# Optimization experiments

Hardware: AMD Instinct MI355X
Metric: run time of the kernel (lower is better)

## Reference

```python
import jax, jax.numpy as jnp
import numpy as np

B_SZ, L_SEQ = 8, 2048
D_MODEL, N_STATE = 1024, 64
NUM_HEADS, N_REC = 1, 8
H_DIM = D_MODEL // NUM_HEADS


def setup_inputs() -> dict:
    key = jax.random.key(0)
    ks = jax.random.split(key, 12)
    Np = N_STATE
    return {
        "u": jax.random.normal(ks[0], (B_SZ, L_SEQ, D_MODEL), jnp.float32),
        "k_proj_w": jax.random.normal(ks[1], (D_MODEL, D_MODEL), jnp.float32) / np.float32(np.sqrt(D_MODEL)),
        "k_proj_b": jax.random.normal(ks[2], (D_MODEL,), jnp.float32) * 0.02,
        "shift_B": jax.random.normal(ks[3], (D_MODEL, Np), jnp.float32) / np.float32(np.sqrt(Np)),
        "shift_C": jax.random.normal(ks[4], (D_MODEL, Np), jnp.float32) / np.float32(np.sqrt(Np)),
        "ssm_k_D": jax.random.normal(ks[5], (D_MODEL,), jnp.float32),
        "log_dt": jax.random.uniform(ks[6], (H_DIM,), jnp.float32, minval=np.float32(np.log(1e-3)), maxval=np.float32(np.log(1e-1))),
        "log_A_real": jnp.log(0.5 * jnp.ones((H_DIM, Np), jnp.float32)),
        "A_imag": jnp.broadcast_to(np.float32(np.pi) * jnp.arange(Np, dtype=jnp.float32), (H_DIM, Np)),
        "B_re": jax.random.normal(ks[7], (H_DIM, Np), jnp.float32),
        "B_im": jax.random.normal(ks[8], (H_DIM, Np), jnp.float32),
    }


def _shift_kernel(Bp, Cp, L):
    # Shift-SSM kernel (SSKernel mode='shift'): K(l) = sum_m C[m+l] * B[m], zero for l >= N.
    N = Bp.shape[-1]
    nfft = 2 * N
    Bf = jnp.fft.rfft(Bp, n=nfft)
    Cf = jnp.fft.rfft(Cp, n=nfft)
    k = jnp.fft.irfft(Cf * jnp.conj(Bf), n=nfft)[..., :N]  # (D, N) linear cross-correlation
    return jnp.pad(k, ((0, 0), (0, L - N)))  # (D, L)


def _kernel_expand(k, log_dt, log_A_real, A_imag, B_re, B_im):
    # Diagonal-SSM state expansion: SSM states x_t = sum_{s<=t} dA^{t-s} dB u_s,
    # read out at N_REC evenly spaced chunk boundaries.
    # k: (B, G, H, L) real -> (B, N_REC, G, H, N) real
    Bb, G, H, L = k.shape
    Lc = L // N_REC
    dt = jnp.exp(log_dt)[:, None]                      # (H,1)
    A = -jnp.exp(log_A_real) + 1j * A_imag             # (H,N)
    dA_log = dt * A                                    # (H,N)
    dB = (B_re + 1j * B_im) * ((jnp.exp(dA_log) - 1.0) / A)  # ZOH discretization
    exps = jnp.arange(Lc - 1, -1, -1, dtype=jnp.float32)      # (Lc,)
    P = jnp.exp(dA_log[..., None] * exps) * dB[..., None]     # (H,N,Lc): dA^{Lc-1-i} dB
    kc = k.reshape(Bb, G, H, N_REC, Lc).astype(P.dtype)
    contrib = jnp.einsum('hnl,bghrl->rbghn', P, kc)           # (N_REC,B,G,H,N)
    dA_Lc = jnp.exp(dA_log * Lc)                              # (H,N)
    x0 = jnp.zeros((Bb, G, H, A.shape[-1]), P.dtype)

    def step(x, c):
        x = dA_Lc * x + c
        return x, x

    _, states = jax.lax.scan(step, x0, contrib)               # (N_REC,B,G,H,N)
    return jnp.transpose(states.real, (1, 0, 2, 3, 4))


def reference(u, k_proj_w, k_proj_b, shift_B, shift_C, ssm_k_D, log_dt, log_A_real, A_imag, B_re, B_im):
    Bb, L, D = u.shape
    # k = W @ u^T + b  -> (B, D, L)
    k = jnp.einsum('bld,hd->bhl', u, k_proj_w) + k_proj_b[None, :, None]
    Ks = _shift_kernel(shift_B, shift_C, L)  # (D, L)
    nfft = 2 * L  # fft_size = L_kernel + L
    conv = jnp.fft.irfft(jnp.fft.rfft(Ks, n=nfft)[None] * jnp.fft.rfft(k, n=nfft), n=nfft)[..., :L]
    k = conv + ssm_k_D[None, :, None] * k
    # rearrange 'b (h d1) l -> b d1 h l'
    k = k.reshape(Bb, H_DIM, NUM_HEADS, L).transpose(0, 2, 1, 3)
    return _kernel_expand(k, log_dt, log_A_real, A_imag, B_re, B_im)
```

## Files before the change

kernel.cpp:

```cpp
#include <hip/hip_runtime.h>
#include <cstddef>
#include <cstdint>

#define L_SEQ 2048
#define DM    1024
#define NREC  8
#define BM 128
#define BN 128
#define BK 32
#define NT (DM / BK)

typedef __attribute__((ext_vector_type(8))) short short8;
typedef __attribute__((ext_vector_type(4))) float f32x4;
typedef __attribute__((ext_vector_type(2))) unsigned int u32x2;

__device__ inline unsigned short f2bf(float f) {
    unsigned u = __float_as_uint(f);
    unsigned r = (u + 0x7FFFu + ((u >> 16) & 1u)) >> 16;
    return (unsigned short)r;
}
__device__ inline float bf2f(unsigned short s) {
    return __uint_as_float(((unsigned)s) << 16);
}
__device__ inline void gload_lds16(const void* g, void* l) {
    __builtin_amdgcn_global_load_lds(
        (const __attribute__((address_space(1))) void*)g,
        (__attribute__((address_space(3))) void*)l, 16, 0, 0);
}

__global__ __launch_bounds__(256) void cvt2_bf16(
    const float* __restrict__ a, unsigned short* __restrict__ oa, int na,
    const float* __restrict__ b, unsigned short* __restrict__ ob, int nb)
{
    int i = (blockIdx.x * 256 + threadIdx.x) * 8;
    const float* src;
    unsigned short* dst;
    if (i < na) { src = a + i; dst = oa + i; }
    else {
        int j = i - na;
        if (j >= nb) return;
        src = b + j; dst = ob + j;
    }
    f32x4 v0 = *(const f32x4*)(src);
    f32x4 v1 = *(const f32x4*)(src + 4);
    short8 o;
    o[0] = (short)f2bf(v0[0]); o[1] = (short)f2bf(v0[1]);
    o[2] = (short)f2bf(v0[2]); o[3] = (short)f2bf(v0[3]);
    o[4] = (short)f2bf(v1[0]); o[5] = (short)f2bf(v1[1]);
    o[6] = (short)f2bf(v1[2]); o[7] = (short)f2bf(v1[3]);
    *(short8*)dst = o;
}

template<bool PREW>
__global__ __launch_bounds__(256, 2) void gemm_klin(
    const float* __restrict__ Wf, const unsigned short* __restrict__ Wb,
    const unsigned short* __restrict__ ub,
    const float* __restrict__ bias, unsigned short* __restrict__ klin)
{
    __shared__ unsigned short As[2][BM * BK];
    __shared__ unsigned short Bs[2][BM * BK];
    int wg = (int)blockIdx.x;
    wg = (wg & 7) * 128 + (wg >> 3);
    const int b  = wg >> 7;
    const int h0 = ((wg >> 4) & 7) * BM;
    const int l0 = (wg & 15) * BN;
    const int tid = threadIdx.x;
    const int lane = tid & 63, wv = tid >> 6;

    const int l3 = lane >> 3, l7 = lane & 7;
    const int g  = l7 ^ l3;
    const int rij  = l3 * 2 + (g >> 2);
    const int kcol = (g & 3) * 8;

    const int rA0 = 2 * wv * 16 + rij;
    const unsigned short* gA0b = Wb + (size_t)(h0 + rA0) * DM + kcol;
    const unsigned short* gA1b = gA0b + 16 * DM;
    const unsigned short* gB0 = ub + ((size_t)(b * L_SEQ + l0 + rA0)) * DM + kcol;
    const unsigned short* gB1 = gB0 + 16 * DM;

    const int r0 = wv * 32 + (lane >> 2);
    const int r1 = r0 + 16;
    const int slotF = lane & 3;
    const float* gA0f = Wf + (size_t)(h0 + r0) * DM + slotF * 8;
    const float* gA1f = Wf + (size_t)(h0 + r1) * DM + slotF * 8;
    const int w0off = (r0 >> 1) * 128 + ((((r0 & 1) << 2) + slotF) ^ ((r0 >> 1) & 7)) * 16;
    const int w1off = (r1 >> 1) * 128 + ((((r1 & 1) << 2) + slotF) ^ ((r1 >> 1) & 7)) * 16;

    const int wm = wv >> 1, wn = wv & 1;
    const int lr = lane & 15, lk = lane >> 4;
    const int foff = (lr >> 1) * 128 + ((((lr & 1) << 2) + lk) ^ (lr >> 1)) * 16;

    f32x4 acc[4][4];
    #pragma unroll
    for (int m = 0; m < 4; ++m)
        #pragma unroll
        for (int n = 0; n < 4; ++n) acc[m][n] = (f32x4){0.f, 0.f, 0.f, 0.f};

    gload_lds16(gB0, &Bs[0][(2 * wv) * 512]);
    gload_lds16(gB1, &Bs[0][(2 * wv + 1) * 512]);
    if constexpr (PREW) {
        gload_lds16(gA0b, &As[0][(2 * wv) * 512]);
        gload_lds16(gA1b, &As[0][(2 * wv + 1) * 512]);
    } else {
        f32x4 a0 = *(const f32x4*)(gA0f);
        f32x4 a1 = *(const f32x4*)(gA0f + 4);
        f32x4 a2 = *(const f32x4*)(gA1f);
        f32x4 a3 = *(const f32x4*)(gA1f + 4);
        short8 c0, c1;
        c0[0]=(short)f2bf(a0[0]); c0[1]=(short)f2bf(a0[1]); c0[2]=(short)f2bf(a0[2]); c0[3]=(short)f2bf(a0[3]);
        c0[4]=(short)f2bf(a1[0]); c0[5]=(short)f2bf(a1[1]); c0[6]=(short)f2bf(a1[2]); c0[7]=(short)f2bf(a1[3]);
        c1[0]=(short)f2bf(a2[0]); c1[1]=(short)f2bf(a2[1]); c1[2]=(short)f2bf(a2[2]); c1[3]=(short)f2bf(a2[3]);
        c1[4]=(short)f2bf(a3[0]); c1[5]=(short)f2bf(a3[1]); c1[6]=(short)f2bf(a3[2]); c1[7]=(short)f2bf(a3[3]);
        *(short8*)((char*)&As[0][0] + w0off) = c0;
        *(short8*)((char*)&As[0][0] + w1off) = c1;
    }

    for (int kt = 0; kt < NT; ++kt) {
        __syncthreads();
        const int bf = kt & 1;
        const bool more = (kt + 1 < NT);
        f32x4 a0, a1, a2, a3;
        if (more) {
            const int ko = (kt + 1) * BK;
            gload_lds16(gB0 + ko, &Bs[bf ^ 1][(2 * wv) * 512]);
            gload_lds16(gB1 + ko, &Bs[bf ^ 1][(2 * wv + 1) * 512]);
            if constexpr (PREW) {
                gload_lds16(gA0b + ko, &As[bf ^ 1][(2 * wv) * 512]);
                gload_lds16(gA1b + ko, &As[bf ^ 1][(2 * wv + 1) * 512]);
            } else {
                a0 = *(const f32x4*)(gA0f + ko);
                a1 = *(const f32x4*)(gA0f + ko + 4);
                a2 = *(const f32x4*)(gA1f + ko);
                a3 = *(const f32x4*)(gA1f + ko + 4);
            }
        }
        short8 af[4], bfr[4];
        #pragma unroll
        for (int m = 0; m < 4; ++m) {
            const int rb = wm * 64 + m * 16;
            af[m] = *(const short8*)((const char*)&As[bf][0] + rb * 64 + foff);
        }
        #pragma unroll
        for (int n = 0; n < 4; ++n) {
            const int rb = wn * 64 + n * 16;
            bfr[n] = *(const short8*)((const char*)&Bs[bf][0] + rb * 64 + foff);
        }
        #pragma unroll
        for (int m = 0; m < 4; ++m)
            #pragma unroll
            for (int n = 0; n < 4; ++n)
                acc[m][n] = __builtin_amdgcn_mfma_f32_16x16x32_bf16(af[m], bfr[n], acc[m][n], 0, 0, 0);
        if constexpr (!PREW) {
            if (more) {
                short8 c0, c1;
                c0[0]=(short)f2bf(a0[0]); c0[1]=(short)f2bf(a0[1]); c0[2]=(short)f2bf(a0[2]); c0[3]=(short)f2bf(a0[3]);
                c0[4]=(short)f2bf(a1[0]); c0[5]=(short)f2bf(a1[1]); c0[6]=(short)f2bf(a1[2]); c0[7]=(short)f2bf(a1[3]);
                c1[0]=(short)f2bf(a2[0]); c1[1]=(short)f2bf(a2[1]); c1[2]=(short)f2bf(a2[2]); c1[3]=(short)f2bf(a2[3]);
                c1[4]=(short)f2bf(a3[0]); c1[5]=(short)f2bf(a3[1]); c1[6]=(short)f2bf(a3[2]); c1[7]=(short)f2bf(a3[3]);
                *(short8*)((char*)&As[bf ^ 1][0] + w0off) = c0;
                *(short8*)((char*)&As[bf ^ 1][0] + w1off) = c1;
            }
        }
    }

    #pragma unroll
    for (int m = 0; m < 4; ++m) {
        const int h = h0 + wm * 64 + m * 16 + lk * 4;
        #pragma unroll
        for (int n = 0; n < 4; ++n) {
            const int l = l0 + wn * 64 + n * 16 + lr;
            #pragma unroll
            for (int r = 0; r < 4; ++r) {
                float v = acc[m][n][r] + bias[h + r];
                klin[((size_t)b * DM + h + r) * L_SEQ + l] = f2bf(v);
            }
        }
    }
}

__device__ inline void get_disc(const float* __restrict__ log_dt,
                                const float* __restrict__ lar,
                                const float* __restrict__ aim, int h, int n,
                                float& Are, float& Aim, float& lre, float& lim)
{
    float dtv = expf(log_dt[h]);
    Are = -expf(lar[h * 64 + n]);
    Aim = aim[h * 64 + n];
    lre = dtv * Are;
    lim = dtv * Aim;
}

__global__ __launch_bounds__(256, 5) void expand(
    const unsigned short* __restrict__ klin,
    const float* __restrict__ shift_B, const float* __restrict__ shift_C,
    const float* __restrict__ ssm_k_D, const float* __restrict__ log_dt,
    const float* __restrict__ log_A_real, const float* __restrict__ A_imag,
    const float* __restrict__ B_re, const float* __restrict__ B_im,
    float* __restrict__ out)
{
    __shared__ __align__(16) char sm[29696];
    constexpr int OKL = 0;
    constexpr int OKK = 8704;
    constexpr int OAF = 16896;
    constexpr int OPR = 20224;
    constexpr int OPI = 24320;
    constexpr int OF  = 28416;
    constexpr int OBS = 28672;
    constexpr int OCS = 28928;
    constexpr int OW32 = 29184;

    const int h  = blockIdx.x;
    const int bg = blockIdx.y;
    const int t = threadIdx.x;
    const int lane = t & 63, wv = t >> 6;

    if (t < 32) {
        int rl = t >> 4, reg = (t >> 3) & 1, idx = t & 7;
        *(f32x4*)&sm[OKL + rl * 4352 + reg * 4224 + idx * 16] = (f32x4){0.f, 0.f, 0.f, 0.f};
    }
    {
        const int rl = wv >> 1, hf = wv & 1;
        const int b = bg * 2 + rl;
        const char* krow = (const char*)(klin + ((size_t)b * DM + h) * L_SEQ);
        const int s = (2 * rl + 1 + (lane >> 3)) & 7;
        const int so = hf * 2048 + (lane >> 3) * 128 + ((lane ^ s) & 7) * 16;
        gload_lds16(krow + so,        &sm[OKL + rl * 4352 + 128 + hf * 2048]);
        gload_lds16(krow + so + 1024, &sm[OKL + rl * 4352 + 128 + hf * 2048 + 1024]);
    }
    if (t < 64) {
        ((float*)&sm[OBS])[t] = shift_B[h * 64 + t];
        ((float*)&sm[OCS])[t] = shift_C[h * 64 + t];
        float Are, Aim, lre, lim;
        get_disc(log_dt, log_A_real, A_imag, h, t, Are, Aim, lre, lim);
        float er = expf(32.f * lre);
        float sn, cs; sincosf(32.f * lim, &sn, &cs);
        ((float*)&sm[OW32])[t * 2]     = er * cs;
        ((float*)&sm[OW32])[t * 2 + 1] = er * sn;
    }
    {
        int n = t >> 2, s4 = t & 3;
        float Are, Aim, lre, lim;
        get_disc(log_dt, log_A_real, A_imag, h, n, Are, Aim, lre, lim);
        float erw = expf(lre), snw, csw;
        sincosf(lim, &snw, &csw);
        float wr = erw * csw, wi = erw * snw;
        float e0 = (float)(24 - 8 * s4);
        float mag = expf(e0 * lre);
        float sn0, cs0; sincosf(e0 * lim, &sn0, &cs0);
        float pr = mag * cs0, pi = mag * sn0;
        float vr[8], vi[8];
        vr[7] = pr; vi[7] = pi;
        #pragma unroll
        for (int k = 6; k >= 0; --k) {
            float nr = pr * wr - pi * wi;
            pi = fmaf(pr, wi, pi * wr);
            pr = nr;
            vr[k] = pr; vi[k] = pi;
        }
        short8 re8, im8;
        #pragma unroll
        for (int e = 0; e < 8; ++e) {
            re8[e] = (short)f2bf(vr[e]);
            im8[e] = (short)f2bf(vi[e]);
        }
        *(short8*)&sm[OPR + t * 16] = re8;
        *(short8*)&sm[OPI + t * 16] = im8;
    }
    __syncthreads();

    if (t < 64) {
        const float* Bp = (const float*)&sm[OBS];
        const float* Cp = (const float*)&sm[OCS];
        float f = (t == 0) ? ssm_k_D[h] : 0.f;
        #pragma unroll 8
        for (int j = 0; j < 64; ++j) {
            float cv = Cp[(j + t) & 63];
            f = fmaf((j + t < 64) ? cv : 0.f, Bp[j], f);
        }
        ((float*)&sm[OF])[t] = f;
    }
    __syncthreads();

    {
        int i = t >> 4, ks = t & 15;
        if (ks < 12) {
            const float* Fp = (const float*)&sm[OF];
            short8 row;
            #pragma unroll
            for (int e = 0; e < 8; ++e) {
                int k = ks * 8 + e;
                int m = 64 + i - k;
                float v = (m >= 0 && m < 64) ? Fp[m] : 0.f;
                row[e] = (short)f2bf(v);
            }
            *(short8*)&sm[OAF + i * 208 + ks * 16] = row;
        }
    }
    __syncthreads();

    {
        short8 afr[3];
        #pragma unroll
        for (int ks = 0; ks < 3; ++ks)
            afr[ks] = *(const short8*)&sm[OAF + (lane & 15) * 208 + ks * 64 + (lane >> 4) * 16];
        const int rl = wv >> 1;
        const int jbase = (wv & 1) * 4;
        #pragma unroll
        for (int jj = 0; jj < 4; ++jj) {
            const int jg = jbase + jj;
            f32x4 d = (f32x4){0.f, 0.f, 0.f, 0.f};
            #pragma unroll
            for (int ks = 0; ks < 3; ++ks) {
                int o = rl * 4352 + (jg * 256 + (lane & 15) * 16 + ks * 32 + (lane >> 4) * 8) * 2;
                o ^= ((o >> 7) & 7) << 4;
                short8 bfrag = *(const short8*)&sm[OKL + o];
                d = __builtin_amdgcn_mfma_f32_16x16x32_bf16(afr[ks], bfrag, d, 0, 0, 0);
            }
            unsigned pk0 = ((unsigned)f2bf(d[0])) | (((unsigned)f2bf(d[1])) << 16);
            unsigned pk1 = ((unsigned)f2bf(d[2])) | (((unsigned)f2bf(d[3])) << 16);
            int o2 = rl * 4096 + jg * 512 + (lane & 15) * 32 + (lane >> 4) * 8;
            o2 ^= ((o2 >> 9) & 7) << 4;
            *(u32x2*)&sm[OKK + o2] = (u32x2){pk0, pk1};
        }
    }
    __syncthreads();

    {
        const int mt = wv;
        short8 par = *(const short8*)&sm[OPR + (mt * 16 + (lane & 15)) * 64 + (lane >> 4) * 16];
        short8 pai = *(const short8*)&sm[OPI + (mt * 16 + (lane & 15)) * 64 + (lane >> 4) * 16];
        float w32r[4], w32i[4];
        #pragma unroll
        for (int rg = 0; rg < 4; ++rg) {
            int n = mt * 16 + (lane >> 4) * 4 + rg;
            float2 ww = *(const float2*)&sm[OW32 + n * 8];
            w32r[rg] = ww.x;
            w32i[rg] = ww.y;
        }
        f32x4 cr = (f32x4){0.f, 0.f, 0.f, 0.f};
        f32x4 ci_ = (f32x4){0.f, 0.f, 0.f, 0.f};
        const int colb = (lane & 15) >> 3;
        const int colr = lane & 7;
        #pragma unroll
        for (int g2 = 0; g2 < 8; ++g2) {
            int o = colb * 4096 + colr * 512 + g2 * 64 + (lane >> 4) * 16;
            o ^= ((o >> 9) & 7) << 4;
            short8 kf = *(const short8*)&sm[OKK + o];
            f32x4 sre = __builtin_amdgcn_mfma_f32_16x16x32_bf16(par, kf, (f32x4){0.f,0.f,0.f,0.f}, 0, 0, 0);
            f32x4 sim = __builtin_amdgcn_mfma_f32_16x16x32_bf16(pai, kf, (f32x4){0.f,0.f,0.f,0.f}, 0, 0, 0);
            #pragma unroll
            for (int rg = 0; rg < 4; ++rg) {
                float wr = w32r[rg], wi = w32i[rg];
                float ncr = fmaf(cr[rg], wr, fmaf(-ci_[rg], wi, sre[rg]));
                float nci = fmaf(cr[rg], wi, fmaf(ci_[rg], wr, sim[rg]));
                cr[rg] = ncr;
                ci_[rg] = nci;
            }
        }
        __syncthreads();
        #pragma unroll
        for (int rg = 0; rg < 4; ++rg) {
            int n = mt * 16 + (lane >> 4) * 4 + rg;
            int c = lane & 15;
            ((float*)&sm[OKK])[n * 17 + c] = cr[rg];
            ((float*)&sm[OKK])[1088 + n * 17 + c] = ci_[rg];
        }
    }
    __syncthreads();

    if (t < 128) {
        const int n = t & 63, bl = t >> 6;
        const int b = bg * 2 + bl;
        float Are, Aim, lre, lim;
        get_disc(log_dt, log_A_real, A_imag, h, n, Are, Aim, lre, lim);
        float er = expf(lre), sn, cs;
        sincosf(lim, &sn, &cs);
        float wr = er * cs, wi = er * sn;
        float2 w32v = *(const float2*)&sm[OW32 + n * 8];
        float ar = w32v.x, ai = w32v.y;
        #pragma unroll
        for (int s = 0; s < 3; ++s) {
            float nr = ar * ar - ai * ai;
            ai = 2.f * ar * ai;
            ar = nr;
        }
        float den = Are * Are + Aim * Aim;
        float wm1r = wr - 1.f, wm1i = wi;
        float tr_ = (wm1r * Are + wm1i * Aim) / den;
        float ti_ = (wm1i * Are - wm1r * Aim) / den;
        float br = B_re[h * 64 + n], bi = B_im[h * 64 + n];
        float dBr = br * tr_ - bi * ti_;
        float dBi = br * ti_ + bi * tr_;
        const float* cre = (const float*)&sm[OKK] + n * 17 + bl * 8;
        const float* cim = (const float*)&sm[OKK] + 1088 + n * 17 + bl * 8;
        float sr = 0.f, si_ = 0.f;
        #pragma unroll
        for (int r = 0; r < 8; ++r) {
            float nsr = fmaf(ar, sr, fmaf(-ai, si_, cre[r]));
            float nsi = fmaf(ar, si_, fmaf(ai, sr, cim[r]));
            sr = nsr; si_ = nsi;
            out[(((size_t)b * NREC + r) * DM + h) * 64 + n] = dBr * sr - dBi * si_;
        }
    }
}

extern "C" void kernel_launch(void* const* d_in, const int* in_sizes, int n_in,
                              void* d_out, int out_size, void* d_ws, size_t ws_size,
                              hipStream_t stream)
{
    const float* u       = (const float*)d_in[0];
    const float* W       = (const float*)d_in[1];
    const float* bias    = (const float*)d_in[2];
    const float* shift_B = (const float*)d_in[3];
    const float* shift_C = (const float*)d_in[4];
    const float* ssm_k_D = (const float*)d_in[5];
    const float* log_dt  = (const float*)d_in[6];
    const float* log_Ar  = (const float*)d_in[7];
    const float* A_imag  = (const float*)d_in[8];
    const float* B_re    = (const float*)d_in[9];
    const float* B_im    = (const float*)d_in[10];
    float* out = (float*)d_out;

    const int n_u = 8 * L_SEQ * DM;
    const int n_w = DM * DM;
    unsigned short* ub   = (unsigned short*)d_ws;
    unsigned short* klin = ub + (size_t)n_u;
    unsigned short* Wb   = klin + (size_t)n_u;

    const bool prew = ws_size >= (size_t)66 * 1024 * 1024;

    if (prew) {
        cvt2_bf16<<<(n_u + n_w) / (256 * 8), 256, 0, stream>>>(u, ub, n_u, W, Wb, n_w);
        gemm_klin<true><<<dim3(1024), 256, 0, stream>>>(W, Wb, ub, bias, klin);
    } else {
        cvt2_bf16<<<n_u / (256 * 8), 256, 0, stream>>>(u, ub, n_u, W, Wb, 0);
        gemm_klin<false><<<dim3(1024), 256, 0, stream>>>(W, Wb, ub, bias, klin);
    }

    expand<<<dim3(DM, 4), 256, 0, stream>>>(klin, shift_B, shift_C, ssm_k_D, log_dt,
                                            log_Ar, A_imag, B_re, B_im, out);
}
```

Before: 87.53 us.

## Add 256x256-tile 8-wave GEMM with 4-stage LDS pipeline for projection

Replaces the 128x128 tile, 4-wave, double-buffered bf16 GEMM with a 256x256 tile, 512-thread kernel. The new kernel uses a four-buffer LDS ring with loads issued three tiles ahead, explicit vmcnt waits and barriers, and s_setprio around the MFMA blocks. Larger tiles raise reuse per loaded byte and the deeper pipeline hides global latency. In exchange, only 256 workgroups launch (one wave of CUs), with 128 KB of LDS and higher register pressure per block. The fallback path for a small workspace is kept as a separate fp32-W kernel.

Measured after the change: 81.88 us. -6.4%, faster.

```diff
diff --git a/kernel.cpp b/kernel.cpp
--- a/kernel.cpp
+++ b/kernel.cpp
@@ -51,9 +51,117 @@
     *(short8*)dst = o;
 }
 
-template<bool PREW>
-__global__ __launch_bounds__(256, 2) void gemm_klin(
-    const float* __restrict__ Wf, const unsigned short* __restrict__ Wb,
+__global__ __launch_bounds__(512, 2) void gemm_klin8(
+    const unsigned short* __restrict__ Wb,
+    const unsigned short* __restrict__ ub,
+    const float* __restrict__ bias, unsigned short* __restrict__ klin)
+{
+    __shared__ unsigned short As[4][256 * 32];
+    __shared__ unsigned short Bs[4][256 * 32];
+
+    int wg = (int)blockIdx.x;
+    wg = (wg & 7) * 32 + (wg >> 3);
+    const int b  = wg >> 5;
+    const int l0 = ((wg >> 2) & 7) * 256;
+    const int h0 = (wg & 3) * 256;
+    const int tid = (int)threadIdx.x;
+    const int lane = tid & 63, wv = tid >> 6;
+
+    const int l3 = lane >> 3, l7 = lane & 7;
+    const int gsw  = l7 ^ l3;
+    const int rij  = l3 * 2 + (gsw >> 2);
+    const int kcol = (gsw & 3) * 8;
+    const int rA0  = wv * 16 + rij;
+
+    const unsigned short* gA0 = Wb + (size_t)(h0 + rA0) * DM + kcol;
+    const unsigned short* gA1 = gA0 + (size_t)128 * DM;
+    const unsigned short* gB0 = ub + ((size_t)b * L_SEQ + l0 + rA0) * DM + kcol;
+    const unsigned short* gB1 = gB0 + (size_t)128 * DM;
+    const int dst0 = (wv * 8) * 128;
+    const int dst1 = (64 + wv * 8) * 128;
+
+    const int wm = wv >> 2, wn = wv & 3;
+    const int lr = lane & 15, lk = lane >> 4;
+    const int foff = (lr >> 1) * 128 + ((((lr & 1) << 2) + lk) ^ (lr >> 1)) * 16;
+
+    f32x4 acc[8][4];
+    #pragma unroll
+    for (int mf = 0; mf < 8; ++mf)
+        #pragma unroll
+        for (int nf = 0; nf < 4; ++nf) acc[mf][nf] = (f32x4){0.f, 0.f, 0.f, 0.f};
+
+#define STG_A(T, BUF) do { const int ko_ = (T) * 32; \
+    gload_lds16(gA0 + ko_, (char*)&As[BUF][0] + dst0); \
+    gload_lds16(gA1 + ko_, (char*)&As[BUF][0] + dst1); } while (0)
+#define STG_B(T, BUF) do { const int ko_ = (T) * 32; \
+    gload_lds16(gB0 + ko_, (char*)&Bs[BUF][0] + dst0); \
+    gload_lds16(gB1 + ko_, (char*)&Bs[BUF][0] + dst1); } while (0)
+
+    STG_A(0, 0); STG_B(0, 0);
+    STG_A(1, 1); STG_B(1, 1);
+    STG_A(2, 2); STG_B(2, 2);
+    asm volatile("s_waitcnt vmcnt(8)" ::: "memory");
+    __builtin_amdgcn_s_barrier();
+    asm volatile("" ::: "memory");
+
+    #pragma unroll 1
+    for (int t = 0; t < 32; ++t) {
+        const int cur = t & 3, st = (t + 3) & 3;
+        const char* Ab = (const char*)&As[cur][0];
+        const char* Bb = (const char*)&Bs[cur][0];
+        short8 af[4], bfr[4];
+        #pragma unroll
+        for (int nf = 0; nf < 4; ++nf)
+            bfr[nf] = *(const short8*)(Bb + (wn * 64 + nf * 16) * 64 + foff);
+        #pragma unroll
+        for (int mf = 0; mf < 4; ++mf)
+            af[mf] = *(const short8*)(Ab + (wm * 128 + mf * 16) * 64 + foff);
+        if (t + 3 < 32) STG_A(t + 3, st);
+        __builtin_amdgcn_s_setprio(1);
+        #pragma unroll
+        for (int mf = 0; mf < 4; ++mf)
+            #pragma unroll
+            for (int nf = 0; nf < 4; ++nf)
+                acc[mf][nf] = __builtin_amdgcn_mfma_f32_16x16x32_bf16(af[mf], bfr[nf], acc[mf][nf], 0, 0, 0);
+        __builtin_amdgcn_s_setprio(0);
+        #pragma unroll
+        for (int mf = 0; mf < 4; ++mf)
+            af[mf] = *(const short8*)(Ab + (wm * 128 + (mf + 4) * 16) * 64 + foff);
+        if (t + 3 < 32) STG_B(t + 3, st);
+        __builtin_amdgcn_s_setprio(1);
+        #pragma unroll
+        for (int mf = 0; mf < 4; ++mf)
+            #pragma unroll
+            for (int nf = 0; nf < 4; ++nf)
+                acc[mf + 4][nf] = __builtin_amdgcn_mfma_f32_16x16x32_bf16(af[mf], bfr[nf], acc[mf + 4][nf], 0, 0, 0);
+        __builtin_amdgcn_s_setprio(0);
+        if (t <= 28)      asm volatile("s_waitcnt vmcnt(8)" ::: "memory");
+        else if (t == 29) asm volatile("s_waitcnt vmcnt(4)" ::: "memory");
+        else              asm volatile("s_waitcnt vmcnt(0)" ::: "memory");
+        __builtin_amdgcn_s_barrier();
+        asm volatile("" ::: "memory");
+        __builtin_amdgcn_sched_barrier(0);
+    }
+#undef STG_A
+#undef STG_B
+
+    #pragma unroll
+    for (int mf = 0; mf < 8; ++mf) {
+        const int h = h0 + wm * 128 + mf * 16 + lk * 4;
+        #pragma unroll
+        for (int nf = 0; nf < 4; ++nf) {
+            const int l = l0 + wn * 64 + nf * 16 + lr;
+            #pragma unroll
+            for (int r = 0; r < 4; ++r) {
+                float v = acc[mf][nf][r] + bias[h + r];
+                klin[((size_t)b * DM + h + r) * L_SEQ + l] = f2bf(v);
+            }
+        }
+    }
+}
+
+__global__ __launch_bounds__(256, 2) void gemm_klin_fb(
+    const float* __restrict__ Wf,
     const unsigned short* __restrict__ ub,
     const float* __restrict__ bias, unsigned short* __restrict__ klin)
 {
@@ -71,10 +179,7 @@
     const int g  = l7 ^ l3;
     const int rij  = l3 * 2 + (g >> 2);
     const int kcol = (g & 3) * 8;
-
     const int rA0 = 2 * wv * 16 + rij;
-    const unsigned short* gA0b = Wb + (size_t)(h0 + rA0) * DM + kcol;
-    const unsigned short* gA1b = gA0b + 16 * DM;
     const unsigned short* gB0 = ub + ((size_t)(b * L_SEQ + l0 + rA0)) * DM + kcol;
     const unsigned short* gB1 = gB0 + 16 * DM;
 
@@ -98,10 +203,7 @@
 
     gload_lds16(gB0, &Bs[0][(2 * wv) * 512]);
     gload_lds16(gB1, &Bs[0][(2 * wv + 1) * 512]);
-    if constexpr (PREW) {
-        gload_lds16(gA0b, &As[0][(2 * wv) * 512]);
-        gload_lds16(gA1b, &As[0][(2 * wv + 1) * 512]);
-    } else {
+    {
         f32x4 a0 = *(const f32x4*)(gA0f);
         f32x4 a1 = *(const f32x4*)(gA0f + 4);
         f32x4 a2 = *(const f32x4*)(gA1f);
@@ -124,15 +226,10 @@
             const int ko = (kt + 1) * BK;
             gload_lds16(gB0 + ko, &Bs[bf ^ 1][(2 * wv) * 512]);
             gload_lds16(gB1 + ko, &Bs[bf ^ 1][(2 * wv + 1) * 512]);
-            if constexpr (PREW) {
-                gload_lds16(gA0b + ko, &As[bf ^ 1][(2 * wv) * 512]);
-                gload_lds16(gA1b + ko, &As[bf ^ 1][(2 * wv + 1) * 512]);
-            } else {
-                a0 = *(const f32x4*)(gA0f + ko);
-                a1 = *(const f32x4*)(gA0f + ko + 4);
-                a2 = *(const f32x4*)(gA1f + ko);
-                a3 = *(const f32x4*)(gA1f + ko + 4);
-            }
+            a0 = *(const f32x4*)(gA0f + ko);
+            a1 = *(const f32x4*)(gA0f + ko + 4);
+            a2 = *(const f32x4*)(gA1f + ko);
+            a3 = *(const f32x4*)(gA1f + ko + 4);
         }
         short8 af[4], bfr[4];
         #pragma unroll
@@ -150,16 +247,14 @@
             #pragma unroll
             for (int n = 0; n < 4; ++n)
                 acc[m][n] = __builtin_amdgcn_mfma_f32_16x16x32_bf16(af[m], bfr[n], acc[m][n], 0, 0, 0);
-        if constexpr (!PREW) {
-            if (more) {
-                short8 c0, c1;
-                c0[0]=(short)f2bf(a0[0]); c0[1]=(short)f2bf(a0[1]); c0[2]=(short)f2bf(a0[2]); c0[3]=(short)f2bf(a0[3]);
-                c0[4]=(short)f2bf(a1[0]); c0[5]=(short)f2bf(a1[1]); c0[6]=(short)f2bf(a1[2]); c0[7]=(short)f2bf(a1[3]);
-                c1[0]=(short)f2bf(a2[0]); c1[1]=(short)f2bf(a2[1]); c1[2]=(short)f2bf(a2[2]); c1[3]=(short)f2bf(a2[3]);
-                c1[4]=(short)f2bf(a3[0]); c1[5]=(short)f2bf(a3[1]); c1[6]=(short)f2bf(a3[2]); c1[7]=(short)f2bf(a3[3]);
-                *(short8*)((char*)&As[bf ^ 1][0] + w0off) = c0;
-                *(short8*)((char*)&As[bf ^ 1][0] + w1off) = c1;
-            }
+        if (more) {
+            short8 c0, c1;
+            c0[0]=(short)f2bf(a0[0]); c0[1]=(short)f2bf(a0[1]); c0[2]=(short)f2bf(a0[2]); c0[3]=(short)f2bf(a0[3]);
+            c0[4]=(short)f2bf(a1[0]); c0[5]=(short)f2bf(a1[1]); c0[6]=(short)f2bf(a1[2]); c0[7]=(short)f2bf(a1[3]);
+            c1[0]=(short)f2bf(a2[0]); c1[1]=(short)f2bf(a2[1]); c1[2]=(short)f2bf(a2[2]); c1[3]=(short)f2bf(a2[3]);
+            c1[4]=(short)f2bf(a3[0]); c1[5]=(short)f2bf(a3[1]); c1[6]=(short)f2bf(a3[2]); c1[7]=(short)f2bf(a3[3]);
+            *(short8*)((char*)&As[bf ^ 1][0] + w0off) = c0;
+            *(short8*)((char*)&As[bf ^ 1][0] + w1off) = c1;
         }
     }
 
@@ -431,10 +526,10 @@
 
     if (prew) {
         cvt2_bf16<<<(n_u + n_w) / (256 * 8), 256, 0, stream>>>(u, ub, n_u, W, Wb, n_w);
-        gemm_klin<true><<<dim3(1024), 256, 0, stream>>>(W, Wb, ub, bias, klin);
+        gemm_klin8<<<dim3(256), 512, 0, stream>>>(Wb, ub, bias, klin);
     } else {
         cvt2_bf16<<<n_u / (256 * 8), 256, 0, stream>>>(u, ub, n_u, W, Wb, 0);
-        gemm_klin<false><<<dim3(1024), 256, 0, stream>>>(W, Wb, ub, bias, klin);
+        gemm_klin_fb<<<dim3(1024), 256, 0, stream>>>(W, ub, bias, klin);
     }
 
     expand<<<dim3(DM, 4), 256, 0, stream>>>(klin, shift_B, shift_C, ssm_k_D, log_dt,
```

## Fuse fp32-to-bf16 conversion into GEMM with larger 256x256 tiles

Applied to the files above, without the earlier changes.

Removes the separate conversion kernel that wrote a bf16 copy of u and W, and instead loads fp32 directly in the GEMM, packing to bf16 in registers before storing to LDS. The GEMM tile grows to 256x256 with 512 threads and 256 blocks, and the MFMA phases are wrapped in s_setprio. This removes a full read/write pass over u, but the GEMM now reads twice the bytes per element from global memory. With only 256 blocks and higher register use, occupancy may not cover all CUs well.

After: 78.16 us. 10.7% less time.

```diff
diff --git a/kernel.cpp b/kernel.cpp
--- a/kernel.cpp
+++ b/kernel.cpp
@@ -5,10 +5,6 @@
 #define L_SEQ 2048
 #define DM    1024
 #define NREC  8
-#define BM 128
-#define BN 128
-#define BK 32
-#define NT (DM / BK)
 
 typedef __attribute__((ext_vector_type(8))) short short8;
 typedef __attribute__((ext_vector_type(4))) float f32x4;
@@ -27,151 +23,120 @@
         (const __attribute__((address_space(1))) void*)g,
         (__attribute__((address_space(3))) void*)l, 16, 0, 0);
 }
-
-__global__ __launch_bounds__(256) void cvt2_bf16(
-    const float* __restrict__ a, unsigned short* __restrict__ oa, int na,
-    const float* __restrict__ b, unsigned short* __restrict__ ob, int nb)
-{
-    int i = (blockIdx.x * 256 + threadIdx.x) * 8;
-    const float* src;
-    unsigned short* dst;
-    if (i < na) { src = a + i; dst = oa + i; }
-    else {
-        int j = i - na;
-        if (j >= nb) return;
-        src = b + j; dst = ob + j;
-    }
-    f32x4 v0 = *(const f32x4*)(src);
-    f32x4 v1 = *(const f32x4*)(src + 4);
-    short8 o;
-    o[0] = (short)f2bf(v0[0]); o[1] = (short)f2bf(v0[1]);
-    o[2] = (short)f2bf(v0[2]); o[3] = (short)f2bf(v0[3]);
-    o[4] = (short)f2bf(v1[0]); o[5] = (short)f2bf(v1[1]);
-    o[6] = (short)f2bf(v1[2]); o[7] = (short)f2bf(v1[3]);
-    *(short8*)dst = o;
-}
-
-template<bool PREW>
-__global__ __launch_bounds__(256, 2) void gemm_klin(
-    const float* __restrict__ Wf, const unsigned short* __restrict__ Wb,
-    const unsigned short* __restrict__ ub,
+__device__ inline short8 pack8(f32x4 x, f32x4 y) {
+    short8 c;
+    c[0] = (short)f2bf(x[0]); c[1] = (short)f2bf(x[1]);
+    c[2] = (short)f2bf(x[2]); c[3] = (short)f2bf(x[3]);
+    c[4] = (short)f2bf(y[0]); c[5] = (short)f2bf(y[1]);
+    c[6] = (short)f2bf(y[2]); c[7] = (short)f2bf(y[3]);
+    return c;
+}
+
+__global__ __launch_bounds__(512, 2) void gemm_fused(
+    const float* __restrict__ Wf, const float* __restrict__ uf,
     const float* __restrict__ bias, unsigned short* __restrict__ klin)
 {
-    __shared__ unsigned short As[2][BM * BK];
-    __shared__ unsigned short Bs[2][BM * BK];
+    __shared__ unsigned short As[2][256 * 32];
+    __shared__ unsigned short Bs[2][256 * 32];
+
     int wg = (int)blockIdx.x;
-    wg = (wg & 7) * 128 + (wg >> 3);
-    const int b  = wg >> 7;
-    const int h0 = ((wg >> 4) & 7) * BM;
-    const int l0 = (wg & 15) * BN;
-    const int tid = threadIdx.x;
+    wg = (wg & 7) * 32 + (wg >> 3);
+    const int b  = wg >> 5;
+    const int l0 = ((wg >> 2) & 7) * 256;
+    const int h0 = (wg & 3) * 256;
+    const int tid = (int)threadIdx.x;
     const int lane = tid & 63, wv = tid >> 6;
 
-    const int l3 = lane >> 3, l7 = lane & 7;
-    const int g  = l7 ^ l3;
-    const int rij  = l3 * 2 + (g >> 2);
-    const int kcol = (g & 3) * 8;
-
-    const int rA0 = 2 * wv * 16 + rij;
-    const unsigned short* gA0b = Wb + (size_t)(h0 + rA0) * DM + kcol;
-    const unsigned short* gA1b = gA0b + 16 * DM;
-    const unsigned short* gB0 = ub + ((size_t)(b * L_SEQ + l0 + rA0)) * DM + kcol;
-    const unsigned short* gB1 = gB0 + 16 * DM;
-
-    const int r0 = wv * 32 + (lane >> 2);
-    const int r1 = r0 + 16;
-    const int slotF = lane & 3;
-    const float* gA0f = Wf + (size_t)(h0 + r0) * DM + slotF * 8;
-    const float* gA1f = Wf + (size_t)(h0 + r1) * DM + slotF * 8;
-    const int w0off = (r0 >> 1) * 128 + ((((r0 & 1) << 2) + slotF) ^ ((r0 >> 1) & 7)) * 16;
-    const int w1off = (r1 >> 1) * 128 + ((((r1 & 1) << 2) + slotF) ^ ((r1 >> 1) & 7)) * 16;
-
-    const int wm = wv >> 1, wn = wv & 1;
+    const int sr0  = tid >> 2;
+    const int slot = tid & 3;
+    const int sr1  = sr0 + 128;
+    const float* gA0 = Wf + (size_t)(h0 + sr0) * DM + slot * 8;
+    const float* gA1 = Wf + (size_t)(h0 + sr1) * DM + slot * 8;
+    const float* gB0 = uf + ((size_t)b * L_SEQ + l0 + sr0) * DM + slot * 8;
+    const float* gB1 = uf + ((size_t)b * L_SEQ + l0 + sr1) * DM + slot * 8;
+    const int w0off = (sr0 >> 1) * 128 + ((((sr0 & 1) << 2) + slot) ^ ((sr0 >> 1) & 7)) * 16;
+    const int w1off = (sr1 >> 1) * 128 + ((((sr1 & 1) << 2) + slot) ^ ((sr1 >> 1) & 7)) * 16;
+
+    const int wm = wv >> 2, wn = wv & 3;
     const int lr = lane & 15, lk = lane >> 4;
     const int foff = (lr >> 1) * 128 + ((((lr & 1) << 2) + lk) ^ (lr >> 1)) * 16;
 
-    f32x4 acc[4][4];
+    f32x4 acc[8][4];
     #pragma unroll
-    for (int m = 0; m < 4; ++m)
-        #pragma unroll
-        for (int n = 0; n < 4; ++n) acc[m][n] = (f32x4){0.f, 0.f, 0.f, 0.f};
-
-    gload_lds16(gB0, &Bs[0][(2 * wv) * 512]);
-    gload_lds16(gB1, &Bs[0][(2 * wv + 1) * 512]);
-    if constexpr (PREW) {
-        gload_lds16(gA0b, &As[0][(2 * wv) * 512]);
-        gload_lds16(gA1b, &As[0][(2 * wv + 1) * 512]);
-    } else {
-        f32x4 a0 = *(const f32x4*)(gA0f);
-        f32x4 a1 = *(const f32x4*)(gA0f + 4);
-        f32x4 a2 = *(const f32x4*)(gA1f);
-        f32x4 a3 = *(const f32x4*)(gA1f + 4);
-        short8 c0, c1;
-        c0[0]=(short)f2bf(a0[0]); c0[1]=(short)f2bf(a0[1]); c0[2]=(short)f2bf(a0[2]); c0[3]=(short)f2bf(a0[3]);
-        c0[4]=(short)f2bf(a1[0]); c0[5]=(short)f2bf(a1[1]); c0[6]=(short)f2bf(a1[2]); c0[7]=(short)f2bf(a1[3]);
-        c1[0]=(short)f2bf(a2[0]); c1[1]=(short)f2bf(a2[1]); c1[2]=(short)f2bf(a2[2]); c1[3]=(short)f2bf(a2[3]);
-        c1[4]=(short)f2bf(a3[0]); c1[5]=(short)f2bf(a3[1]); c1[6]=(short)f2bf(a3[2]); c1[7]=(short)f2bf(a3[3]);
-        *(short8*)((char*)&As[0][0] + w0off) = c0;
-        *(short8*)((char*)&As[0][0] + w1off) = c1;
-    }
-
-    for (int kt = 0; kt < NT; ++kt) {
-        __syncthreads();
-        const int bf = kt & 1;
-        const bool more = (kt + 1 < NT);
-        f32x4 a0, a1, a2, a3;
-        if (more) {
-            const int ko = (kt + 1) * BK;
-            gload_lds16(gB0 + ko, &Bs[bf ^ 1][(2 * wv) * 512]);
-            gload_lds16(gB1 + ko, &Bs[bf ^ 1][(2 * wv + 1) * 512]);
-            if constexpr (PREW) {
-                gload_lds16(gA0b + ko, &As[bf ^ 1][(2 * wv) * 512]);
-                gload_lds16(gA1b + ko, &As[bf ^ 1][(2 * wv + 1) * 512]);
-            } else {
-                a0 = *(const f32x4*)(gA0f + ko);
-                a1 = *(const f32x4*)(gA0f + ko + 4);
-                a2 = *(const f32x4*)(gA1f + ko);
-                a3 = *(const f32x4*)(gA1f + ko + 4);
-            }
+    for (int mf = 0; mf < 8; ++mf)
+        #pragma unroll
+        for (int nf = 0; nf < 4; ++nf) acc[mf][nf] = (f32x4){0.f, 0.f, 0.f, 0.f};
+
+    {
+        f32x4 a0 = *(const f32x4*)(gA0), a1 = *(const f32x4*)(gA0 + 4);
+        f32x4 a2 = *(const f32x4*)(gA1), a3 = *(const f32x4*)(gA1 + 4);
+        f32x4 b0 = *(const f32x4*)(gB0), b1 = *(const f32x4*)(gB0 + 4);
+        f32x4 b2 = *(const f32x4*)(gB1), b3 = *(const f32x4*)(gB1 + 4);
+        *(short8*)((char*)&As[0][0] + w0off) = pack8(a0, a1);
+        *(short8*)((char*)&As[0][0] + w1off) = pack8(a2, a3);
+        *(short8*)((char*)&Bs[0][0] + w0off) = pack8(b0, b1);
+        *(short8*)((char*)&Bs[0][0] + w1off) = pack8(b2, b3);
+    }
+    __syncthreads();
+
+    #pragma unroll 1
+    for (int t = 0; t < 32; ++t) {
+        const int cur = t & 1;
+        const char* Ab = (const char*)&As[cur][0];
+        const char* Bb = (const char*)&Bs[cur][0];
+        f32x4 a0, a1, a2, a3, b0, b1, b2, b3;
+        if (t < 31) {
+            const int ko = (t + 1) * 32;
+            a0 = *(const f32x4*)(gA0 + ko); a1 = *(const f32x4*)(gA0 + ko + 4);
+            a2 = *(const f32x4*)(gA1 + ko); a3 = *(const f32x4*)(gA1 + ko + 4);
+            b0 = *(const f32x4*)(gB0 + ko); b1 = *(const f32x4*)(gB0 + ko + 4);
+            b2 = *(const f32x4*)(gB1 + ko); b3 = *(const f32x4*)(gB1 + ko + 4);
         }
         short8 af[4], bfr[4];
         #pragma unroll
-        for (int m = 0; m < 4; ++m) {
-            const int rb = wm * 64 + m * 16;
-            af[m] = *(const short8*)((const char*)&As[bf][0] + rb * 64 + foff);
-        }
-        #pragma unroll
-        for (int n = 0; n < 4; ++n) {
-            const int rb = wn * 64 + n * 16;
-            bfr[n] = *(const short8*)((const char*)&Bs[bf][0] + rb * 64 + foff);
-        }
-        #pragma unroll
-        for (int m = 0; m < 4; ++m)
-            #pragma unroll
-            for (int n = 0; n < 4; ++n)
-                acc[m][n] = __builtin_amdgcn_mfma_f32_16x16x32_bf16(af[m], bfr[n], acc[m][n], 0, 0, 0);
-        if constexpr (!PREW) {
-            if (more) {
-                short8 c0, c1;
-                c0[0]=(short)f2bf(a0[0]); c0[1]=(short)f2bf(a0[1]); c0[2]=(short)f2bf(a0[2]); c0[3]=(short)f2bf(a0[3]);
-                c0[4]=(short)f2bf(a1[0]); c0[5]=(short)f2bf(a1[1]); c0[6]=(short)f2bf(a1[2]); c0[7]=(short)f2bf(a1[3]);
-                c1[0]=(short)f2bf(a2[0]); c1[1]=(short)f2bf(a2[1]); c1[2]=(short)f2bf(a2[2]); c1[3]=(short)f2bf(a2[3]);
-                c1[4]=(short)f2bf(a3[0]); c1[5]=(short)f2bf(a3[1]); c1[6]=(short)f2bf(a3[2]); c1[7]=(short)f2bf(a3[3]);
-                *(short8*)((char*)&As[bf ^ 1][0] + w0off) = c0;
-                *(short8*)((char*)&As[bf ^ 1][0] + w1off) = c1;
-            }
+        for (int nf = 0; nf < 4; ++nf)
+            bfr[nf] = *(const short8*)(Bb + (wn * 64 + nf * 16) * 64 + foff);
+        #pragma unroll
+        for (int mf = 0; mf < 4; ++mf)
+            af[mf] = *(const short8*)(Ab + (wm * 128 + mf * 16) * 64 + foff);
+        __builtin_amdgcn_s_setprio(1);
+        #pragma unroll
+        for (int mf = 0; mf < 4; ++mf)
+            #pragma unroll
+            for (int nf = 0; nf < 4; ++nf)
+                acc[mf][nf] = __builtin_amdgcn_mfma_f32_16x16x32_bf16(af[mf], bfr[nf], acc[mf][nf], 0, 0, 0);
+        __builtin_amdgcn_s_setprio(0);
+        #pragma unroll
+        for (int mf = 0; mf < 4; ++mf)
+            af[mf] = *(const short8*)(Ab + (wm * 128 + (mf + 4) * 16) * 64 + foff);
+        __builtin_amdgcn_s_setprio(1);
+        #pragma unroll
+        for (int mf = 0; mf < 4; ++mf)
+            #pragma unroll
+            for (int nf = 0; nf < 4; ++nf)
+                acc[mf + 4][nf] = __builtin_amdgcn_mfma_f32_16x16x32_bf16(af[mf], bfr[nf], acc[mf + 4][nf], 0, 0, 0);
+        __builtin_amdgcn_s_setprio(0);
+        __builtin_amdgcn_sched_barrier(0);
+        if (t < 31) {
+            char* An = (char*)&As[cur ^ 1][0];
+            char* Bn = (char*)&Bs[cur ^ 1][0];
+            *(short8*)(An + w0off) = pack8(a0, a1);
+            *(short8*)(An + w1off) = pack8(a2, a3);
+            *(short8*)(Bn + w0off) = pack8(b0, b1);
+            *(short8*)(Bn + w1off) = pack8(b2, b3);
+            __syncthreads();
         }
     }
 
     #pragma unroll
-    for (int m = 0; m < 4; ++m) {
-        const int h = h0 + wm * 64 + m * 16 + lk * 4;
-        #pragma unroll
-        for (int n = 0; n < 4; ++n) {
-            const int l = l0 + wn * 64 + n * 16 + lr;
+    for (int mf = 0; mf < 8; ++mf) {
+        const int h = h0 + wm * 128 + mf * 16 + lk * 4;
+        #pragma unroll
+        for (int nf = 0; nf < 4; ++nf) {
+            const int l = l0 + wn * 64 + nf * 16 + lr;
             #pragma unroll
             for (int r = 0; r < 4; ++r) {
-                float v = acc[m][n][r] + bias[h + r];
+                float v = acc[mf][nf][r] + bias[h + r];
                 klin[((size_t)b * DM + h + r) * L_SEQ + l] = f2bf(v);
             }
         }
@@ -421,21 +386,9 @@
     const float* B_im    = (const float*)d_in[10];
     float* out = (float*)d_out;
 
-    const int n_u = 8 * L_SEQ * DM;
-    const int n_w = DM * DM;
-    unsigned short* ub   = (unsigned short*)d_ws;
-    unsigned short* klin = ub + (size_t)n_u;
-    unsigned short* Wb   = klin + (size_t)n_u;
-
-    const bool prew = ws_size >= (size_t)66 * 1024 * 1024;
-
-    if (prew) {
-        cvt2_bf16<<<(n_u + n_w) / (256 * 8), 256, 0, stream>>>(u, ub, n_u, W, Wb, n_w);
-        gemm_klin<true><<<dim3(1024), 256, 0, stream>>>(W, Wb, ub, bias, klin);
-    } else {
-        cvt2_bf16<<<n_u / (256 * 8), 256, 0, stream>>>(u, ub, n_u, W, Wb, 0);
-        gemm_klin<false><<<dim3(1024), 256, 0, stream>>>(W, Wb, ub, bias, klin);
-    }
+    unsigned short* klin = (unsigned short*)d_ws;
+
+    gemm_fused<<<dim3(256), 512, 0, stream>>>(W, u, bias, klin);
 
     expand<<<dim3(DM, 4), 256, 0, stream>>>(klin, shift_B, shift_C, ssm_k_D, log_dt,
                                             log_Ar, A_imag, B_re, B_im, out);
```
